# Kernel tuning notes

Measured on AMD Instinct MI355X. Metric: run time of the kernel, lower is better.

Reference implementation:

```python
import jax, jax.numpy as jnp
import numpy as np

N_HEAD = 12
N_EMBD = 768
BLOCK = 4096
B, T = 2, 4096


def setup_inputs() -> dict:
    key = jax.random.key(0)
    k1, k2, k3, k4, k5 = jax.random.split(key, 5)
    s_in = 1.0 / np.sqrt(N_EMBD)
    return {
        "x": jax.random.normal(k1, (B, T, N_EMBD), dtype=jnp.float32),
        "w_attn": jax.random.normal(k2, (N_EMBD, 3 * N_EMBD), dtype=jnp.float32) * s_in,
        "b_attn": jax.random.normal(k3, (3 * N_EMBD,), dtype=jnp.float32) * 0.02,
        "w_proj": jax.random.normal(k4, (N_EMBD, N_EMBD), dtype=jnp.float32) * s_in,
        "b_proj": jax.random.normal(k5, (N_EMBD,), dtype=jnp.float32) * 0.02,
    }


def reference(x, w_attn, b_attn, w_proj, b_proj):
    Bsz, Tlen, C = x.shape
    hd = C // N_HEAD  # head dim = 64
    qkv = x @ w_attn + b_attn                      # [B,T,3C]
    q, k, v = jnp.split(qkv, 3, axis=-1)
    # [B,T,C] -> [B,H,T,hd]
    def heads(t):
        return t.reshape(Bsz, Tlen, N_HEAD, hd).transpose(0, 2, 1, 3)
    q, k, v = heads(q), heads(k), heads(v)
    scale = 1.0 / np.sqrt(hd).astype(np.float32)
    att = jnp.einsum("bhqd,bhkd->bhqk", q, k) * scale  # [B,H,T,T]
    causal = jnp.tril(jnp.ones((Tlen, Tlen), dtype=bool))
    att = jnp.where(causal[None, None, :, :], att, -jnp.inf)
    att = jax.nn.softmax(att, axis=-1)
    y = jnp.einsum("bhqk,bhkd->bhqd", att, v)      # [B,H,T,hd]
    y = y.transpose(0, 2, 1, 3).reshape(Bsz, Tlen, C)
    return y @ w_proj + b_proj
```

## Files before the change

### kernel.cpp

```cpp
#include <hip/hip_runtime.h>


#define DEVFN __device__ __forceinline__

typedef __attribute__((ext_vector_type(8)))  short   short8;
typedef __attribute__((ext_vector_type(4)))  short   short4v;
typedef __attribute__((ext_vector_type(8)))  __bf16  bf16x8;
typedef __attribute__((ext_vector_type(4)))  float   f32x4;
typedef __attribute__((ext_vector_type(16))) float   f32x16;

constexpr int BATCH = 2;
constexpr int T     = 4096;
constexpr int CDIM  = 768;
constexpr int NH    = 12;
constexpr int HD    = 64;
constexpr int M_TOK = BATCH * T;
constexpr int N_QKV = 3 * CDIM;
constexpr int N_QK  = 2 * CDIM;
constexpr float QSCALE = 0.125f * 1.44269504f;

DEVFN short f2bf(float f) {
  unsigned u = __builtin_bit_cast(unsigned, f);
  u += 0x7fffu + ((u >> 16) & 1u);
  return (short)(u >> 16);
}
DEVFN float bf2f(short s) {
  return __builtin_bit_cast(float, ((unsigned)(unsigned short)s) << 16);
}
DEVFN short nbf(float f) {
  return __builtin_bit_cast(short, (__bf16)f);
}
DEVFN unsigned pack2(float a, float b) {
  union { __bf16 h[2]; unsigned u; } x;
  x.h[0] = (__bf16)a; x.h[1] = (__bf16)b;
  return x.u;
}
DEVFN float ex2(float x) { return __builtin_amdgcn_exp2f(x); }
DEVFN void pl32swap(unsigned& a, unsigned& b) {
  asm volatile("v_permlane32_swap_b32 %0, %1" : "+v"(a), "+v"(b));
}
DEVFN f32x4 mfma16(short8 a, short8 b, f32x4 c) {
  return __builtin_amdgcn_mfma_f32_16x16x32_bf16(
      __builtin_bit_cast(bf16x8, a), __builtin_bit_cast(bf16x8, b), c, 0, 0, 0);
}
DEVFN f32x16 mfma32(short8 a, short8 b, f32x16 c) {
  return __builtin_amdgcn_mfma_f32_32x32x16_bf16(
      __builtin_bit_cast(bf16x8, a), __builtin_bit_cast(bf16x8, b), c, 0, 0, 0);
}
DEVFN short8 mk8(unsigned w0, unsigned w1, unsigned w2, unsigned w3) {
  union { unsigned u[4]; short8 s; } x;
  x.u[0] = w0; x.u[1] = w1; x.u[2] = w2; x.u[3] = w3;
  return x.s;
}
DEVFN void gload16(const short* g, short* l) {
  __builtin_amdgcn_global_load_lds(
      (const __attribute__((address_space(1))) void*)g,
      (__attribute__((address_space(3))) void*)l, 16, 0, 0);
}

__global__ void cast_f32_bf16(const float* __restrict__ in,
                              short* __restrict__ out, int n) {
  int i = (blockIdx.x * blockDim.x + threadIdx.x) * 4;
  if (i >= n) return;
  f32x4 v = *reinterpret_cast<const f32x4*>(in + i);
  short4v o;
#pragma unroll
  for (int j = 0; j < 4; ++j) o[j] = f2bf(v[j]);
  *reinterpret_cast<short4v*>(out + i) = o;
}

__global__ void transpose_cast2(const float* __restrict__ wA,
                                const float* __restrict__ wP,
                                short* __restrict__ outA,
                                short* __restrict__ outP) {
  __shared__ float tile[32][33];
  const int R = CDIM;
  int c0g = blockIdx.x * 32, r0 = blockIdx.y * 32;
  const float* in;
  short* out;
  int Cc, c0;
  if (c0g < N_QKV) { in = wA; out = outA; Cc = N_QKV; c0 = c0g; }
  else             { in = wP; out = outP; Cc = CDIM;  c0 = c0g - N_QKV; }
  int tx = threadIdx.x, ty = threadIdx.y;
#pragma unroll
  for (int j = 0; j < 32; j += 8) {
    int r = r0 + ty + j, c = c0 + tx;
    tile[ty + j][tx] = in[(size_t)r * Cc + c];
  }
  __syncthreads();
#pragma unroll
  for (int j = 0; j < 32; j += 8) {
    int r = r0 + tx, c = c0 + ty + j;
    out[(size_t)c * R + r] = f2bf(tile[tx][ty + j]);
  }
}

__global__ void vtrans(const short* __restrict__ v, short* __restrict__ vt) {
  __shared__ short t_lds[64 * 72];
  const int t0 = blockIdx.x * 64;
  const int bh = blockIdx.y;
  const int b = bh / NH, h = bh % NH;
  const int tid = threadIdx.x;
#pragma unroll
  for (int j = 0; j < 2; ++j) {
    int c = j * 256 + tid;
    int tr = c >> 3, dc = (c & 7) << 3;
    short8 vv = *reinterpret_cast<const short8*>(
        v + (size_t)(b * T + t0 + tr) * CDIM + h * HD + dc);
#pragma unroll
    for (int e = 0; e < 8; ++e) t_lds[(dc + e) * 72 + tr] = vv[e];
  }
  __syncthreads();
#pragma unroll
  for (int j = 0; j < 2; ++j) {
    int c = j * 256 + tid;
    int d = c >> 3, tc = (c & 7) << 3;
    short8 o = *reinterpret_cast<const short8*>(&t_lds[d * 72 + tc]);
    *reinterpret_cast<short8*>(vt + (size_t)(bh * HD + d) * T + t0 + tc) = o;
  }
}

template <int MODE>
__global__ __launch_bounds__(256)
void gemm_bt(const short* __restrict__ A, const short* __restrict__ Bt,
             const float* __restrict__ bias, float* __restrict__ Cf,
             short* __restrict__ qk_out, short* __restrict__ v_out,
             int M, int N, int K) {
  constexpr int BM = 128, BK = 64;
  __shared__ short As[BM * BK];
  __shared__ short Bs[BM * BK];
  const int bm = blockIdx.x, bn = blockIdx.y;
  const int tid = threadIdx.x;
  const int lane = tid & 63, wid = tid >> 6;
  const int wm = wid >> 1, wn = wid & 1;
  const int lr = lane & 15, lh = lane >> 4;

  f32x4 acc[4][4] = {};

  const short* Abase = A + (size_t)(bm * BM) * K;
  const short* Bbase = Bt + (size_t)(bn * BM) * K;

  int srow[4], scolS[4];
#pragma unroll
  for (int c = 0; c < 4; ++c) {
    int ck = c * 256 + tid;
    int row = ck >> 3, colB = (ck & 7) << 4;
    srow[c] = row;
    scolS[c] = (colB ^ ((row & 7) << 4)) >> 1;
  }

  for (int k0 = 0; k0 < K; k0 += BK) {
    __syncthreads();
#pragma unroll
    for (int c = 0; c < 4; ++c) {
      gload16(Abase + (size_t)srow[c] * K + k0 + scolS[c],
              &As[(c * 256 + wid * 64) * 8]);
      gload16(Bbase + (size_t)srow[c] * K + k0 + scolS[c],
              &Bs[(c * 256 + wid * 64) * 8]);
    }
    __syncthreads();

#pragma unroll
    for (int kk = 0; kk < 2; ++kk) {
      short8 af[4], bfr[4];
#pragma unroll
      for (int m = 0; m < 4; ++m) {
        int r = wm * 64 + m * 16 + lr;
        int cB = (kk * 64 + lh * 16) ^ ((r & 7) << 4);
        af[m] = *reinterpret_cast<const short8*>(&As[(r * 128 + cB) >> 1]);
      }
#pragma unroll
      for (int n = 0; n < 4; ++n) {
        int r = wn * 64 + n * 16 + lr;
        int cB = (kk * 64 + lh * 16) ^ ((r & 7) << 4);
        bfr[n] = *reinterpret_cast<const short8*>(&Bs[(r * 128 + cB) >> 1]);
      }
#pragma unroll
      for (int m = 0; m < 4; ++m)
#pragma unroll
        for (int n = 0; n < 4; ++n)
          acc[m][n] = mfma16(af[m], bfr[n], acc[m][n]);
    }
  }

#pragma unroll
  for (int m = 0; m < 4; ++m) {
#pragma unroll
    for (int n = 0; n < 4; ++n) {
#pragma unroll
      for (int r = 0; r < 4; ++r) {
        int row = bm * BM + wm * 64 + m * 16 + lh * 4 + r;
        int col = bn * BM + wn * 64 + n * 16 + lr;
        float v = acc[m][n][r] + bias[col];
        if (MODE == 0) {
          Cf[(size_t)row * N + col] = v;
        } else {
          if (bn < 6) {
            qk_out[(size_t)row * N_QK + col] = f2bf(v * QSCALE);
          } else if (bn < 12) {
            qk_out[(size_t)row * N_QK + col] = f2bf(v);
          } else {
            v_out[(size_t)row * CDIM + (col - N_QK)] = f2bf(v);
          }
        }
      }
    }
  }
}

__global__ __launch_bounds__(256, 3)
void attn_kernel(const short* __restrict__ qk, const short* __restrict__ vt,
                 short* __restrict__ y) {
  __shared__ short smem[16384];

  const int blk = blockIdx.x;
  const int xcd = blk & 7, slot = blk >> 3;
  const int bh = xcd * 3 + slot % 3;
  const int qt = 31 - slot / 3;
  const int b = bh / NH, h = bh % NH;
  const int tid = threadIdx.x;
  const int wid = tid >> 6;
  const int lane = tid & 63;
  const int c31 = lane & 31, hi = lane >> 5;

  const short* qk_b  = qk + (size_t)b * T * N_QK;
  const short* vt_bh = vt + (size_t)(bh * HD) * T;

  const short* kp[2];
  const short* vp[2];
  int lsw[2];
#pragma unroll
  for (int c = 0; c < 2; ++c) {
    int ck = c * 256 + tid;
    int row = ck >> 3, colB = (ck & 7) << 4;
    lsw[c] = (row * 128 + (colB ^ ((row & 7) << 4))) >> 1;
    kp[c] = qk_b + (size_t)row * N_QK + CDIM + h * HD + (colB >> 1);
    vp[c] = vt_bh + (size_t)row * T + (colB >> 1);
  }

  const int swq = (c31 & 7) << 4;

  const int wq = qt * 128 + wid * 32;
  const int qabs = wq + c31;

  short8 qf[4];
  {
    const short* qp = qk_b + (size_t)qabs * N_QK + h * HD;
#pragma unroll
    for (int ds = 0; ds < 4; ++ds)
      qf[ds] = *reinterpret_cast<const short8*>(qp + ds * 16 + hi * 8);
  }

  const short8 ones = {0x3F80, 0x3F80, 0x3F80, 0x3F80,
                       0x3F80, 0x3F80, 0x3F80, 0x3F80};

  f32x16 oacc[2], lacc;
#pragma unroll
  for (int dt = 0; dt < 2; ++dt)
#pragma unroll
    for (int r = 0; r < 16; ++r) oacc[dt][r] = 0.f;
#pragma unroll
  for (int r = 0; r < 16; ++r) lacc[r] = 0.f;

  const int nt = 2 * qt + 2;

  short8 kr[2], vr[2];
#pragma unroll
  for (int c = 0; c < 2; ++c) {
    kr[c] = *reinterpret_cast<const short8*>(kp[c]);
    vr[c] = *reinterpret_cast<const short8*>(vp[c]);
  }

  for (int t = 0; t < nt; ++t) {
    short* Kg = smem + (t & 1) * 8192;
    short* Vg = Kg + 4096;
#pragma unroll
    for (int c = 0; c < 2; ++c) {
      *reinterpret_cast<short8*>(&Kg[lsw[c]]) = kr[c];
      *reinterpret_cast<short8*>(&Vg[lsw[c]]) = vr[c];
    }
    __syncthreads();
    if (t + 1 < nt) {
      size_t ko = (size_t)(t + 1) * 64 * N_QK;
      int    vo = (t + 1) * 64;
#pragma unroll
      for (int c = 0; c < 2; ++c) {
        kr[c] = *reinterpret_cast<const short8*>(kp[c] + ko);
        vr[c] = *reinterpret_cast<const short8*>(vp[c] + vo);
      }
    }

    const int ks = t * 64;
    if (ks > wq + 31) continue;

    f32x16 s0, s1;
#pragma unroll
    for (int r = 0; r < 16; ++r) { s0[r] = 0.f; s1[r] = 0.f; }
    __builtin_amdgcn_s_setprio(1);
#pragma unroll
    for (int ds = 0; ds < 4; ++ds) {
      int cB = (ds * 32 + hi * 16) ^ swq;
      short8 kf0 =
          *reinterpret_cast<const short8*>(&Kg[(c31 * 128 + cB) >> 1]);
      short8 kf1 = *reinterpret_cast<const short8*>(
          &Kg[((32 + c31) * 128 + cB) >> 1]);
      s0 = mfma32(kf0, qf[ds], s0);
      s1 = mfma32(kf1, qf[ds], s1);
    }
    __builtin_amdgcn_s_setprio(0);

    if (ks + 63 > wq) {
#pragma unroll
      for (int r = 0; r < 16; ++r) {
        int kab = ks + (r & 3) + 8 * (r >> 2) + 4 * hi;
        if (kab > qabs) s0[r] = -1e30f;
        if (kab + 32 > qabs) s1[r] = -1e30f;
      }
    }

#pragma unroll
    for (int r = 0; r < 16; ++r) s0[r] = ex2(s0[r]);
#pragma unroll
    for (int r = 0; r < 16; ++r) s1[r] = ex2(s1[r]);

#pragma unroll
    for (int KT = 0; KT < 4; ++KT) {
      const f32x16& p = (KT < 2) ? s0 : s1;
      const int bse = (KT & 1) * 8;
      unsigned Aw = pack2(p[bse + 0], p[bse + 1]);
      unsigned Bw = pack2(p[bse + 2], p[bse + 3]);
      unsigned Cw = pack2(p[bse + 4], p[bse + 5]);
      unsigned Dw = pack2(p[bse + 6], p[bse + 7]);
      pl32swap(Aw, Cw);
      pl32swap(Bw, Dw);
      short8 pf = mk8(Aw, Bw, Cw, Dw);
      int cB = (KT * 32 + hi * 16) ^ swq;
      __builtin_amdgcn_s_setprio(1);
#pragma unroll
      for (int dt = 0; dt < 2; ++dt) {
        short8 vf = *reinterpret_cast<const short8*>(
            &Vg[((dt * 32 + c31) * 128 + cB) >> 1]);
        oacc[dt] = mfma32(vf, pf, oacc[dt]);
      }
      lacc = mfma32(ones, pf, lacc);
      __builtin_amdgcn_s_setprio(0);
    }
  }

  float inv = 1.0f / lacc[0];
  short* yp = y + (size_t)(b * T + qabs) * CDIM + h * HD;
#pragma unroll
  for (int dt = 0; dt < 2; ++dt) {
#pragma unroll
    for (int qd = 0; qd < 4; ++qd) {
      short4v o4;
#pragma unroll
      for (int e = 0; e < 4; ++e) o4[e] = nbf(oacc[dt][4 * qd + e] * inv);
      *reinterpret_cast<short4v*>(yp + dt * 32 + qd * 8 + hi * 4) = o4;
    }
  }
}

extern "C" void kernel_launch(void* const* d_in, const int* in_sizes, int n_in,
                              void* d_out, int out_size, void* d_ws,
                              size_t ws_size, hipStream_t stream) {
  const float* x      = (const float*)d_in[0];
  const float* w_attn = (const float*)d_in[1];
  const float* b_attn = (const float*)d_in[2];
  const float* w_proj = (const float*)d_in[3];
  const float* b_proj = (const float*)d_in[4];
  float* out = (float*)d_out;

  short* xb   = (short*)d_ws;
  short* watT = xb + (size_t)M_TOK * CDIM;
  short* wpT  = watT + (size_t)N_QKV * CDIM;
  short* qkB  = wpT + (size_t)CDIM * CDIM;
  short* vB   = qkB + (size_t)M_TOK * N_QK;
  short* vtB  = vB + (size_t)M_TOK * CDIM;
  short* yb   = xb;

  {
    int n = M_TOK * CDIM;
    cast_f32_bf16<<<n / 4 / 256, 256, 0, stream>>>(x, xb, n);
  }
  transpose_cast2<<<dim3(3072 / 32, CDIM / 32), dim3(32, 8), 0, stream>>>(
      w_attn, w_proj, watT, wpT);

  gemm_bt<2><<<dim3(M_TOK / 128, N_QKV / 128), 256, 0, stream>>>(
      xb, watT, b_attn, nullptr, qkB, vB, M_TOK, N_QKV, CDIM);

  vtrans<<<dim3(T / 64, BATCH * NH), 256, 0, stream>>>(vB, vtB);

  attn_kernel<<<dim3(768), 256, 0, stream>>>(qkB, vtB, yb);

  gemm_bt<0><<<dim3(M_TOK / 128, CDIM / 128), 256, 0, stream>>>(
      yb, wpT, b_proj, out, nullptr, nullptr, M_TOK, CDIM, CDIM);
}
```

Before: 165.0 us.

## Fuse prep kernels, shrink GEMM N-tiles, and rebalance attention query-tile order

Merges the x cast and weight transpose-cast into a single prep launch, saving one kernel launch. Templates the GEMM on its N-fragment count so the QKV GEMM uses 96-wide and the projection GEMM 64-wide N tiles, which raises the block count to fill more CUs. The attention block-to-query-tile mapping is reordered to mix heavy and light causal tiles and improve load balance. Smaller N tiles reduce reuse of each A tile and add more A traffic per output.

```diff
diff --git a/kernel.cpp b/kernel.cpp
--- a/kernel.cpp
+++ b/kernel.cpp
@@ -58,30 +58,28 @@
       (__attribute__((address_space(3))) void*)l, 16, 0, 0);
 }
 
-__global__ void cast_f32_bf16(const float* __restrict__ in,
-                              short* __restrict__ out, int n) {
-  int i = (blockIdx.x * blockDim.x + threadIdx.x) * 4;
-  if (i >= n) return;
-  f32x4 v = *reinterpret_cast<const f32x4*>(in + i);
-  short4v o;
-#pragma unroll
-  for (int j = 0; j < 4; ++j) o[j] = f2bf(v[j]);
-  *reinterpret_cast<short4v*>(out + i) = o;
-}
-
-__global__ void transpose_cast2(const float* __restrict__ wA,
-                                const float* __restrict__ wP,
-                                short* __restrict__ outA,
-                                short* __restrict__ outP) {
+__global__ void prep(const float* __restrict__ x, const float* __restrict__ wA,
+                     const float* __restrict__ wP, short* __restrict__ xb,
+                     short* __restrict__ outA, short* __restrict__ outP) {
   __shared__ float tile[32][33];
-  const int R = CDIM;
-  int c0g = blockIdx.x * 32, r0 = blockIdx.y * 32;
+  const int blk = blockIdx.x, tid = threadIdx.x;
+  if (blk < 6144) {
+    int i = (blk * 256 + tid) * 4;
+    f32x4 v = *reinterpret_cast<const f32x4*>(x + i);
+    short4v o;
+#pragma unroll
+    for (int j = 0; j < 4; ++j) o[j] = f2bf(v[j]);
+    *reinterpret_cast<short4v*>(xb + i) = o;
+    return;
+  }
+  const int bid = blk - 6144;
+  const int c0g = (bid % 96) * 32, r0 = (bid / 96) * 32;
   const float* in;
   short* out;
   int Cc, c0;
   if (c0g < N_QKV) { in = wA; out = outA; Cc = N_QKV; c0 = c0g; }
   else             { in = wP; out = outP; Cc = CDIM;  c0 = c0g - N_QKV; }
-  int tx = threadIdx.x, ty = threadIdx.y;
+  const int tx = tid & 31, ty = tid >> 5;
 #pragma unroll
   for (int j = 0; j < 32; j += 8) {
     int r = r0 + ty + j, c = c0 + tx;
@@ -91,7 +89,7 @@
 #pragma unroll
   for (int j = 0; j < 32; j += 8) {
     int r = r0 + tx, c = c0 + ty + j;
-    out[(size_t)c * R + r] = f2bf(tile[tx][ty + j]);
+    out[(size_t)c * CDIM + r] = f2bf(tile[tx][ty + j]);
   }
 }
 
@@ -120,49 +118,57 @@
   }
 }
 
-template <int MODE>
+template <int MODE, int NF>
 __global__ __launch_bounds__(256)
 void gemm_bt(const short* __restrict__ A, const short* __restrict__ Bt,
              const float* __restrict__ bias, float* __restrict__ Cf,
              short* __restrict__ qk_out, short* __restrict__ v_out,
              int M, int N, int K) {
-  constexpr int BM = 128, BK = 64;
+  constexpr int BM = 128, BK = 64, BN = NF * 32;
   __shared__ short As[BM * BK];
-  __shared__ short Bs[BM * BK];
+  __shared__ short Bs[BN * BK];
   const int bm = blockIdx.x, bn = blockIdx.y;
   const int tid = threadIdx.x;
   const int lane = tid & 63, wid = tid >> 6;
   const int wm = wid >> 1, wn = wid & 1;
   const int lr = lane & 15, lh = lane >> 4;
 
-  f32x4 acc[4][4] = {};
+  f32x4 acc[4][NF] = {};
 
   const short* Abase = A + (size_t)(bm * BM) * K;
-  const short* Bbase = Bt + (size_t)(bn * BM) * K;
-
-  int srow[4], scolS[4];
+  const short* Bbase = Bt + (size_t)(bn * BN) * K;
+
+  int srowA[4], scolA[4], srowB[NF], scolB[NF];
 #pragma unroll
   for (int c = 0; c < 4; ++c) {
     int ck = c * 256 + tid;
     int row = ck >> 3, colB = (ck & 7) << 4;
-    srow[c] = row;
-    scolS[c] = (colB ^ ((row & 7) << 4)) >> 1;
+    srowA[c] = row;
+    scolA[c] = (colB ^ ((row & 7) << 4)) >> 1;
+  }
+#pragma unroll
+  for (int c = 0; c < NF; ++c) {
+    int ck = c * 256 + tid;
+    int row = ck >> 3, colB = (ck & 7) << 4;
+    srowB[c] = row;
+    scolB[c] = (colB ^ ((row & 7) << 4)) >> 1;
   }
 
   for (int k0 = 0; k0 < K; k0 += BK) {
     __syncthreads();
 #pragma unroll
-    for (int c = 0; c < 4; ++c) {
-      gload16(Abase + (size_t)srow[c] * K + k0 + scolS[c],
+    for (int c = 0; c < 4; ++c)
+      gload16(Abase + (size_t)srowA[c] * K + k0 + scolA[c],
               &As[(c * 256 + wid * 64) * 8]);
-      gload16(Bbase + (size_t)srow[c] * K + k0 + scolS[c],
+#pragma unroll
+    for (int c = 0; c < NF; ++c)
+      gload16(Bbase + (size_t)srowB[c] * K + k0 + scolB[c],
               &Bs[(c * 256 + wid * 64) * 8]);
-    }
     __syncthreads();
 
 #pragma unroll
     for (int kk = 0; kk < 2; ++kk) {
-      short8 af[4], bfr[4];
+      short8 af[4], bfr[NF];
 #pragma unroll
       for (int m = 0; m < 4; ++m) {
         int r = wm * 64 + m * 16 + lr;
@@ -170,15 +176,15 @@
         af[m] = *reinterpret_cast<const short8*>(&As[(r * 128 + cB) >> 1]);
       }
 #pragma unroll
-      for (int n = 0; n < 4; ++n) {
-        int r = wn * 64 + n * 16 + lr;
+      for (int n = 0; n < NF; ++n) {
+        int r = wn * (BN / 2) + n * 16 + lr;
         int cB = (kk * 64 + lh * 16) ^ ((r & 7) << 4);
         bfr[n] = *reinterpret_cast<const short8*>(&Bs[(r * 128 + cB) >> 1]);
       }
 #pragma unroll
       for (int m = 0; m < 4; ++m)
 #pragma unroll
-        for (int n = 0; n < 4; ++n)
+        for (int n = 0; n < NF; ++n)
           acc[m][n] = mfma16(af[m], bfr[n], acc[m][n]);
     }
   }
@@ -186,18 +192,18 @@
 #pragma unroll
   for (int m = 0; m < 4; ++m) {
 #pragma unroll
-    for (int n = 0; n < 4; ++n) {
+    for (int n = 0; n < NF; ++n) {
 #pragma unroll
       for (int r = 0; r < 4; ++r) {
         int row = bm * BM + wm * 64 + m * 16 + lh * 4 + r;
-        int col = bn * BM + wn * 64 + n * 16 + lr;
+        int col = bn * BN + wn * (BN / 2) + n * 16 + lr;
         float v = acc[m][n][r] + bias[col];
         if (MODE == 0) {
           Cf[(size_t)row * N + col] = v;
         } else {
-          if (bn < 6) {
+          if (col < CDIM) {
             qk_out[(size_t)row * N_QK + col] = f2bf(v * QSCALE);
-          } else if (bn < 12) {
+          } else if (col < N_QK) {
             qk_out[(size_t)row * N_QK + col] = f2bf(v);
           } else {
             v_out[(size_t)row * CDIM + (col - N_QK)] = f2bf(v);
@@ -216,7 +222,14 @@
   const int blk = blockIdx.x;
   const int xcd = blk & 7, slot = blk >> 3;
   const int bh = xcd * 3 + slot % 3;
-  const int qt = 31 - slot / 3;
+  const int qidx = slot / 3;
+  int qt;
+  if (qidx <= 9)       qt = 31 - qidx;
+  else if (qidx <= 20) qt = qidx - 10;
+  else {
+    int k = qidx - 21;
+    qt = (k & 1) ? 17 + (k >> 1) : 16 - (k >> 1);
+  }
   const int b = bh / NH, h = bh % NH;
   const int tid = threadIdx.x;
   const int wid = tid >> 6;
@@ -379,20 +392,16 @@
   short* vtB  = vB + (size_t)M_TOK * CDIM;
   short* yb   = xb;
 
-  {
-    int n = M_TOK * CDIM;
-    cast_f32_bf16<<<n / 4 / 256, 256, 0, stream>>>(x, xb, n);
-  }
-  transpose_cast2<<<dim3(3072 / 32, CDIM / 32), dim3(32, 8), 0, stream>>>(
-      w_attn, w_proj, watT, wpT);
-
-  gemm_bt<2><<<dim3(M_TOK / 128, N_QKV / 128), 256, 0, stream>>>(
+  prep<<<dim3(6144 + 2304), 256, 0, stream>>>(x, w_attn, w_proj, xb, watT,
+                                              wpT);
+
+  gemm_bt<2, 3><<<dim3(M_TOK / 128, N_QKV / 96), 256, 0, stream>>>(
       xb, watT, b_attn, nullptr, qkB, vB, M_TOK, N_QKV, CDIM);
 
   vtrans<<<dim3(T / 64, BATCH * NH), 256, 0, stream>>>(vB, vtB);
 
   attn_kernel<<<dim3(768), 256, 0, stream>>>(qkB, vtB, yb);
 
-  gemm_bt<0><<<dim3(M_TOK / 128, CDIM / 128), 256, 0, stream>>>(
+  gemm_bt<0, 2><<<dim3(M_TOK / 128, CDIM / 64), 256, 0, stream>>>(
       yb, wpT, b_proj, out, nullptr, nullptr, M_TOK, CDIM, CDIM);
 }
```

After: 152.2 us. 7.8% less time.
